# Performance work log

Measured on AMD Instinct MI355X. Metric: run time of the kernel, lower is better.

The kernel has to match this reference:

```python
import jax, jax.numpy as jnp
import numpy as np

BS, N_AGENTS, SA_DIM, HID = 2048, 64, 128, 256


def setup_inputs() -> dict:
    key = jax.random.key(0)
    ks = jax.random.split(key, 16)
    s = lambda fan_in: 1.0 / np.sqrt(fan_in)
    u = lambda k, shp, b: jax.random.uniform(k, shp, jnp.float32, -b, b)
    return {
        "x": jax.random.normal(ks[0], (BS, N_AGENTS, SA_DIM), jnp.float32),
        # encoder: Linear(sa, hid) -> Linear(hid, hid)
        "enc_w1": u(ks[1], (SA_DIM, HID), s(SA_DIM)),
        "enc_b1": u(ks[2], (HID,), s(SA_DIM)),
        "enc_w2": u(ks[3], (HID, HID), s(HID)),
        "enc_b2": u(ks[4], (HID,), s(HID)),
        # attention 'general' linear_in (no bias)
        "attn_w": u(ks[5], (HID, HID), s(HID)),
        # gc1: Linear(sa, hid); nn_gc1: Linear(sa, hid)
        "gc1_w": u(ks[6], (SA_DIM, HID), s(SA_DIM)),
        "gc1_b": u(ks[7], (HID,), s(SA_DIM)),
        "nn1_w": u(ks[8], (SA_DIM, HID), s(SA_DIM)),
        "nn1_b": u(ks[9], (HID,), s(SA_DIM)),
        # gc2: Linear(hid, hid); nn_gc2: Linear(hid, hid)
        "gc2_w": u(ks[10], (HID, HID), s(HID)),
        "gc2_b": u(ks[11], (HID,), s(HID)),
        "nn2_w": u(ks[12], (HID, HID), s(HID)),
        "nn2_b": u(ks[13], (HID,), s(HID)),
        "n_agents": N_AGENTS,
    }


def reference(x, enc_w1, enc_b1, enc_w2, enc_b2, attn_w,
              gc1_w, gc1_b, nn1_w, nn1_b, gc2_w, gc2_b, nn2_w, nn2_b,
              n_agents):
    relu = jax.nn.relu
    inv_n = 1.0 / n_agents
    # encoder MLP: relu(relu(x W1 + b1) W2 + b2)  -> [bs, n, hid]
    emb = relu(relu(x @ enc_w1 + enc_b1) @ enc_w2 + enc_b2)
    # general attention: softmax((emb W_a) emb^T) over last axis -> [bs, n, n]
    scores = jnp.einsum('bnd,bmd->bnm', emb @ attn_w, emb)
    attn = jax.nn.softmax(scores, axis=-1)
    # gc1: adj @ Linear(x); residual relu branch; normalize by n_agents
    feat = relu(jnp.einsum('bnm,bmh->bnh', attn, x @ gc1_w + gc1_b))
    feat = (feat + relu(x @ nn1_w + nn1_b)) * inv_n
    # gc2 on feat
    out = relu(jnp.einsum('bnm,bmh->bnh', attn, feat @ gc2_w + gc2_b))
    out = (out + relu(feat @ nn2_w + nn2_b)) * inv_n
    return out, attn
```

## Files before the change

kernel.cpp:

```cpp
#include <hip/hip_runtime.h>

typedef _Float16 half8 __attribute__((ext_vector_type(8)));
typedef _Float16 half4_t __attribute__((ext_vector_type(4)));
typedef float f32x4 __attribute__((ext_vector_type(4)));

#define NBATCH 2048
#define NA 64
#define SA 128
#define HID 256

#define OFF_X 0
#define OFF_R0 8192
#define OFF_ATT (8192 + 16384)
#define SMEM_BYTES ((8192 + 16384 + 8192) * 2)

#define W_ENC1 0
#define W_ENC2 (W_ENC1 + 128 * 256)
#define W_ATTN (W_ENC2 + 256 * 256)
#define W_GC1 (W_ATTN + 256 * 256)
#define W_NN1 (W_GC1 + 128 * 256)
#define W_GC2 (W_NN1 + 128 * 256)
#define W_NN2 (W_GC2 + 256 * 256)

#define MFMA(a, b, cacc) __builtin_amdgcn_mfma_f32_16x16x32_f16((a), (b), (cacc), 0, 0, 0)

#define BAR()                                            \
  do {                                                   \
    asm volatile("s_waitcnt lgkmcnt(0)" ::: "memory");   \
    __builtin_amdgcn_s_barrier();                        \
  } while (0)

__global__ void pack_all(const float* __restrict__ e1, const float* __restrict__ e2,
                         const float* __restrict__ aw, const float* __restrict__ g1,
                         const float* __restrict__ n1, const float* __restrict__ g2,
                         const float* __restrict__ n2, _Float16* __restrict__ dst) {
  int b = (int)blockIdx.x;
  const float* src;
  int off;
  if (b < 16) { src = e1; off = W_ENC1; }
  else if (b < 48) { src = e2; off = W_ENC2; b -= 16; }
  else if (b < 80) { src = aw; off = W_ATTN; b -= 48; }
  else if (b < 96) { src = g1; off = W_GC1; b -= 80; }
  else if (b < 112) { src = n1; off = W_NN1; b -= 96; }
  else if (b < 144) { src = g2; off = W_GC2; b -= 112; }
  else { src = n2; off = W_NN2; b -= 144; }
  int t = b * 256 + (int)threadIdx.x;
  int lane = t & 63, frag = t >> 6;
  int nt = frag & 15, kt = frag >> 4;
  int g = lane >> 4, c = lane & 15;
  half8 h;
#pragma unroll
  for (int j = 0; j < 8; ++j)
    h[j] = (_Float16)src[(size_t)(kt * 32 + g * 8 + j) * 256 + nt * 16 + c];
  *(half8*)(dst + off + (size_t)t * 8) = h;
}

__global__ __launch_bounds__(256, 2) void dicg_main(
    const float* __restrict__ x, const float* __restrict__ b_enc1,
    const float* __restrict__ b_enc2, const float* __restrict__ b_gc1,
    const float* __restrict__ b_nn1, const float* __restrict__ b_gc2,
    const float* __restrict__ b_nn2, const _Float16* __restrict__ wp,
    float* __restrict__ out, float* __restrict__ attn_out) {
  extern __shared__ _Float16 sm[];
  _Float16* X = sm + OFF_X;
  _Float16* R0 = sm + OFF_R0;
  _Float16* ATTp = sm + OFF_ATT;

  const int tid = (int)threadIdx.x;
  const int wv = tid >> 6;
  const int lane = tid & 63;
  const int g = lane >> 4;
  const int c = lane & 15;
  const int bb = (int)blockIdx.x;
  const float* __restrict__ xb = x + (size_t)bb * (NA * SA);

  auto ldA = [&](const _Float16* p, int kt, int rt) -> half8 {
    return *(const half8*)(p + (kt * 4 + rt) * 512 + lane * 8);
  };
  auto ldB = [&](const _Float16* p, int kt, int ct) -> half8 {
    return *(const half8*)(p + (kt * 16 + ct) * 512 + lane * 8);
  };
  auto wfrag = [&](const _Float16* wb, int kt, int ntg) -> half8 {
    return *(const half8*)(wb + ((size_t)(kt * 16 + ntg) * 64 + lane) * 8);
  };
  auto xfrag = [&](int r0, int k0) -> half8 {
    const float* p = xb + (r0 + c) * SA + k0 + g * 8;
    f32x4 u = *(const f32x4*)p;
    f32x4 v = *(const f32x4*)(p + 4);
    half8 h;
    h[0] = (_Float16)u[0]; h[1] = (_Float16)u[1];
    h[2] = (_Float16)u[2]; h[3] = (_Float16)u[3];
    h[4] = (_Float16)v[0]; h[5] = (_Float16)v[1];
    h[6] = (_Float16)v[2]; h[7] = (_Float16)v[3];
    return h;
  };

  auto stA_val = [&](_Float16* dst, int rt, int nt, int r, float v) {
    int kt = 2 * wv + (nt >> 1);
    int lanep = (2 * (nt & 1) + (c >> 3)) * 16 + 4 * g + r;
    dst[(kt * 4 + rt) * 512 + lanep * 8 + (c & 7)] = (_Float16)v;
  };
  auto ep_storeA = [&](f32x4(&acc)[4][4], const float* bias, bool dorelu) {
#pragma unroll
    for (int nt = 0; nt < 4; ++nt) {
      float bv = bias[64 * wv + 16 * nt + c];
#pragma unroll
      for (int rt = 0; rt < 4; ++rt)
#pragma unroll
        for (int r = 0; r < 4; ++r) {
          float y = acc[rt][nt][r] + bv;
          if (dorelu) y = fmaxf(y, 0.f);
          stA_val(R0, rt, nt, r, y);
        }
    }
  };
  auto ep_storeB = [&](f32x4(&acc)[4][4], const float* bias) {
#pragma unroll
    for (int nt = 0; nt < 4; ++nt) {
      float bv = bias[64 * wv + 16 * nt + c];
#pragma unroll
      for (int rt = 0; rt < 4; ++rt) {
        half4_t h;
#pragma unroll
        for (int r = 0; r < 4; ++r) h[r] = (_Float16)(acc[rt][nt][r] + bv);
        int fi = (rt >> 1) * 16 + 4 * wv + nt;
        int lanep = (2 * (rt & 1) + (g >> 1)) * 16 + c;
        *(half4_t*)(R0 + fi * 512 + lanep * 8 + 4 * (g & 1)) = h;
      }
    }
  };
  auto stQ = [&](const f32x4(&q2)[2], int s) {
    _Float16* base = ATTp + (8 + 2 * wv + s) * 512;
#pragma unroll
    for (int nt2 = 0; nt2 < 2; ++nt2)
#pragma unroll
      for (int r = 0; r < 4; ++r)
        base[((2 * nt2 + (c >> 3)) * 16 + 4 * g + r) * 8 + (c & 7)] = (_Float16)q2[nt2][r];
  };
  auto mm_att = [&](f32x4(&acc)[4][4]) {
#pragma unroll
    for (int kt = 0; kt < 2; ++kt) {
      half8 af[4], bf[4];
#pragma unroll
      for (int rt = 0; rt < 4; ++rt) af[rt] = ldA(ATTp, kt, rt);
#pragma unroll
      for (int nt = 0; nt < 4; ++nt) bf[nt] = ldB(R0, kt, 4 * wv + nt);
#pragma unroll
      for (int rt = 0; rt < 4; ++rt)
#pragma unroll
        for (int nt = 0; nt < 4; ++nt) acc[rt][nt] = MFMA(af[rt], bf[nt], acc[rt][nt]);
    }
  };

  half8 pf2[4][4];
  half8 pfq[8][2];
  half8 pf5g[2][4], pf5n[2][4];
  half8 pf7n[3][4], pf7g[3][4];

  {
    f32x4 acc[4][4]{};
#pragma unroll
    for (int kt = 0; kt < 4; ++kt) {
      half8 af[4], bf[4];
#pragma unroll
      for (int rt = 0; rt < 4; ++rt) af[rt] = xfrag(16 * rt, kt * 32);
#pragma unroll
      for (int nt = 0; nt < 4; ++nt) bf[nt] = wfrag(wp + W_ENC1, kt, 4 * wv + nt);
      if (kt == wv) {
#pragma unroll
        for (int rt = 0; rt < 4; ++rt)
          *(half8*)(X + (kt * 4 + rt) * 512 + lane * 8) = af[rt];
      }
#pragma unroll
      for (int rt = 0; rt < 4; ++rt)
#pragma unroll
        for (int nt = 0; nt < 4; ++nt) acc[rt][nt] = MFMA(af[rt], bf[nt], acc[rt][nt]);
    }
#pragma unroll
    for (int s = 0; s < 4; ++s)
#pragma unroll
      for (int nt = 0; nt < 4; ++nt) pf2[s][nt] = wfrag(wp + W_ENC2, s, 4 * wv + nt);
    ep_storeA(acc, b_enc1, true);
  }
  BAR();
  {
    f32x4 acc[4][4]{};
#pragma unroll
    for (int kt = 0; kt < 8; ++kt) {
      half8 af[4], bf[4];
#pragma unroll
      for (int rt = 0; rt < 4; ++rt) af[rt] = ldA(R0, kt, rt);
#pragma unroll
      for (int nt = 0; nt < 4; ++nt)
        bf[nt] = (kt < 4) ? pf2[kt][nt] : wfrag(wp + W_ENC2, kt, 4 * wv + nt);
#pragma unroll
      for (int rt = 0; rt < 4; ++rt)
#pragma unroll
        for (int nt = 0; nt < 4; ++nt) acc[rt][nt] = MFMA(af[rt], bf[nt], acc[rt][nt]);
    }
#pragma unroll
    for (int k2 = 0; k2 < 8; ++k2) {
      pfq[k2][0] = wfrag(wp + W_ATTN, k2, 0);
      pfq[k2][1] = wfrag(wp + W_ATTN, k2, 1);
    }
    BAR();
    ep_storeA(acc, b_enc2, true);
  }
  BAR();
  {
    half8 aeK[8];
#pragma unroll
    for (int k2 = 0; k2 < 8; ++k2) aeK[k2] = ldA(R0, k2, wv);
    f32x4 sc[4]{};
    {
      f32x4 q2[2]{};
#pragma unroll
      for (int k2 = 0; k2 < 8; ++k2) {
        q2[0] = MFMA(aeK[k2], pfq[k2][0], q2[0]);
        q2[1] = MFMA(aeK[k2], pfq[k2][1], q2[1]);
      }
      stQ(q2, 0);
    }
#pragma unroll
    for (int ktp = 0; ktp < 8; ++ktp) {
      f32x4 q2n[2]{};
      if (ktp < 7) {
#pragma unroll
        for (int k2 = 0; k2 < 8; ++k2) {
          q2n[0] = MFMA(aeK[k2], wfrag(wp + W_ATTN, k2, 2 * ktp + 2), q2n[0]);
          q2n[1] = MFMA(aeK[k2], wfrag(wp + W_ATTN, k2, 2 * ktp + 3), q2n[1]);
        }
      }
      asm volatile("s_waitcnt lgkmcnt(0)" ::: "memory");
      half8 qb = *(const half8*)(ATTp + (8 + 2 * wv + (ktp & 1)) * 512 + lane * 8);
      if (ktp < 7) stQ(q2n, (ktp + 1) & 1);
#pragma unroll
      for (int rt = 0; rt < 4; ++rt) sc[rt] = MFMA(ldA(R0, ktp, rt), qb, sc[rt]);
    }
    float m = sc[0][0];
#pragma unroll
    for (int rt = 0; rt < 4; ++rt)
#pragma unroll
      for (int r = 0; r < 4; ++r) m = fmaxf(m, sc[rt][r]);
    m = fmaxf(m, __shfl_xor(m, 16));
    m = fmaxf(m, __shfl_xor(m, 32));
    float e[4][4], s = 0.f;
#pragma unroll
    for (int rt = 0; rt < 4; ++rt)
#pragma unroll
      for (int r = 0; r < 4; ++r) {
        e[rt][r] = __expf(sc[rt][r] - m);
        s += e[rt][r];
      }
    s += __shfl_xor(s, 16);
    s += __shfl_xor(s, 32);
    float inv = 1.0f / s;
#pragma unroll
    for (int s5 = 0; s5 < 2; ++s5)
#pragma unroll
      for (int nt = 0; nt < 4; ++nt) {
        pf5g[s5][nt] = wfrag(wp + W_GC1, s5, 4 * wv + nt);
        pf5n[s5][nt] = wfrag(wp + W_NN1, s5, 4 * wv + nt);
      }
    float* ao = attn_out + ((size_t)bb * NA + 16 * wv + c) * NA;
#pragma unroll
    for (int rt = 0; rt < 4; ++rt) {
      f32x4 vv;
      half4_t hh;
#pragma unroll
      for (int r = 0; r < 4; ++r) {
        vv[r] = e[rt][r] * inv;
        hh[r] = (_Float16)vv[r];
      }
      *(f32x4*)(ao + 16 * rt + 4 * g) = vv;
      int fi = (rt >> 1) * 4 + wv;
      int lanep = (2 * (rt & 1) + (g >> 1)) * 16 + c;
      *(half4_t*)(ATTp + fi * 512 + lanep * 8 + 4 * (g & 1)) = hh;
    }
  }
  BAR();
  half4_t r1h[4][4];
  {
    f32x4 aG[4][4]{}, aN[4][4]{};
#pragma unroll
    for (int kt = 0; kt < 4; ++kt) {
      half8 af[4], b1[4], b2[4];
#pragma unroll
      for (int rt = 0; rt < 4; ++rt) af[rt] = ldA(X, kt, rt);
#pragma unroll
      for (int nt = 0; nt < 4; ++nt)
        b1[nt] = (kt < 2) ? pf5g[kt][nt] : wfrag(wp + W_GC1, kt, 4 * wv + nt);
#pragma unroll
      for (int nt = 0; nt < 4; ++nt)
        b2[nt] = (kt < 2) ? pf5n[kt][nt] : wfrag(wp + W_NN1, kt, 4 * wv + nt);
#pragma unroll
      for (int rt = 0; rt < 4; ++rt)
#pragma unroll
        for (int nt = 0; nt < 4; ++nt) {
          aG[rt][nt] = MFMA(af[rt], b1[nt], aG[rt][nt]);
          aN[rt][nt] = MFMA(af[rt], b2[nt], aN[rt][nt]);
        }
    }
    ep_storeB(aG, b_gc1);
#pragma unroll
    for (int nt = 0; nt < 4; ++nt) {
      float bv = b_nn1[64 * wv + 16 * nt + c];
#pragma unroll
      for (int rt = 0; rt < 4; ++rt)
#pragma unroll
        for (int r = 0; r < 4; ++r)
          r1h[rt][nt][r] = (_Float16)fmaxf(aN[rt][nt][r] + bv, 0.f);
    }
#pragma unroll
    for (int s2 = 0; s2 < 2; ++s2)
#pragma unroll
      for (int nt = 0; nt < 4; ++nt) {
        pf7n[s2][nt] = wfrag(wp + W_NN2, s2, 4 * wv + nt);
        pf7g[s2][nt] = wfrag(wp + W_GC2, s2, 4 * wv + nt);
      }
  }
  BAR();
  {
#pragma unroll
    for (int nt = 0; nt < 4; ++nt) {
      pf7n[2][nt] = wfrag(wp + W_NN2, 2, 4 * wv + nt);
      pf7g[2][nt] = wfrag(wp + W_GC2, 2, 4 * wv + nt);
    }
    f32x4 a1[4][4]{};
    mm_att(a1);
    BAR();
#pragma unroll
    for (int nt = 0; nt < 4; ++nt)
#pragma unroll
      for (int rt = 0; rt < 4; ++rt)
#pragma unroll
        for (int r = 0; r < 4; ++r)
          stA_val(R0, rt, nt, r,
                  (fmaxf(a1[rt][nt][r], 0.f) + (float)r1h[rt][nt][r]) * 0.015625f);
  }
  BAR();
  half4_t r2h[4][4];
  {
    f32x4 aN2[4][4]{}, aG2[4][4]{};
#pragma unroll
    for (int kt = 0; kt < 8; ++kt) {
      half8 af[4], b1[4], b2[4];
#pragma unroll
      for (int rt = 0; rt < 4; ++rt) af[rt] = ldA(R0, kt, rt);
#pragma unroll
      for (int nt = 0; nt < 4; ++nt)
        b1[nt] = (kt < 3) ? pf7n[kt][nt] : wfrag(wp + W_NN2, kt, 4 * wv + nt);
#pragma unroll
      for (int nt = 0; nt < 4; ++nt)
        b2[nt] = (kt < 3) ? pf7g[kt][nt] : wfrag(wp + W_GC2, kt, 4 * wv + nt);
#pragma unroll
      for (int rt = 0; rt < 4; ++rt)
#pragma unroll
        for (int nt = 0; nt < 4; ++nt) {
          aN2[rt][nt] = MFMA(af[rt], b1[nt], aN2[rt][nt]);
          aG2[rt][nt] = MFMA(af[rt], b2[nt], aG2[rt][nt]);
        }
    }
#pragma unroll
    for (int nt = 0; nt < 4; ++nt) {
      float bv = b_nn2[64 * wv + 16 * nt + c];
#pragma unroll
      for (int rt = 0; rt < 4; ++rt)
#pragma unroll
        for (int r = 0; r < 4; ++r)
          r2h[rt][nt][r] = (_Float16)fmaxf(aN2[rt][nt][r] + bv, 0.f);
    }
    BAR();
    ep_storeB(aG2, b_gc2);
  }
  BAR();
  {
    f32x4 a1[4][4]{};
    mm_att(a1);
    float* ob = out + (size_t)bb * NA * HID;
#pragma unroll
    for (int nt = 0; nt < 4; ++nt)
#pragma unroll
      for (int rt = 0; rt < 4; ++rt)
#pragma unroll
        for (int r = 0; r < 4; ++r)
          ob[(size_t)(16 * rt + 4 * g + r) * HID + 64 * wv + 16 * nt + c] =
              (fmaxf(a1[rt][nt][r], 0.f) + (float)r2h[rt][nt][r]) * 0.015625f;
  }
}

extern "C" void kernel_launch(void* const* d_in, const int* in_sizes, int n_in,
                              void* d_out, int out_size, void* d_ws, size_t ws_size,
                              hipStream_t stream) {
  const float* x = (const float*)d_in[0];
  const float* enc_w1 = (const float*)d_in[1];
  const float* enc_b1 = (const float*)d_in[2];
  const float* enc_w2 = (const float*)d_in[3];
  const float* enc_b2 = (const float*)d_in[4];
  const float* attn_w = (const float*)d_in[5];
  const float* gc1_w = (const float*)d_in[6];
  const float* gc1_b = (const float*)d_in[7];
  const float* nn1_w = (const float*)d_in[8];
  const float* nn1_b = (const float*)d_in[9];
  const float* gc2_w = (const float*)d_in[10];
  const float* gc2_b = (const float*)d_in[11];
  const float* nn2_w = (const float*)d_in[12];
  const float* nn2_b = (const float*)d_in[13];

  _Float16* wp = (_Float16*)d_ws;
  float* out = (float*)d_out;
  float* attn_o = out + (size_t)NBATCH * NA * HID;

  pack_all<<<176, 256, 0, stream>>>(enc_w1, enc_w2, attn_w, gc1_w, nn1_w, gc2_w,
                                    nn2_w, wp);
  dicg_main<<<NBATCH, 256, SMEM_BYTES, stream>>>(
      x, enc_b1, enc_b2, gc1_b, nn1_b, gc2_b, nn2_b, wp, out, attn_o);
}
```

Measured before the change: 154.6 us.

## Compute attention-aggregation outputs transposed to vectorize stores and drop barriers

Swaps MFMA operand order for the gc1/gc2 attention products and the nn residual branches so each lane holds four consecutive hidden columns. Feature tiles can then be written with half4 stores into a transposed LDS layout (read back via a new ldFeat), and the final output uses 16-byte float4 global stores instead of scalar ones. Two block barriers are removed, on the assumption that the new layout lets each wave write only its own region. This aims to cut scattered LDS and global stores and synchronization. It risks read/write races in R0 if the removed barriers were still needed.

Result: no change. 156.3 us (+1.1%).

```diff
diff --git a/kernel.cpp b/kernel.cpp
--- a/kernel.cpp
+++ b/kernel.cpp
@@ -80,6 +80,9 @@
   auto ldB = [&](const _Float16* p, int kt, int ct) -> half8 {
     return *(const half8*)(p + (kt * 16 + ct) * 512 + lane * 8);
   };
+  auto ldFeat = [&](int kt, int rt) -> half8 {
+    return *(const half8*)(R0 + ((kt & 1) * 16 + 4 * (kt >> 1) + rt) * 512 + lane * 8);
+  };
   auto wfrag = [&](const _Float16* wb, int kt, int ntg) -> half8 {
     return *(const half8*)(wb + ((size_t)(kt * 16 + ntg) * 64 + lane) * 8);
   };
@@ -129,6 +132,11 @@
       }
     }
   };
+  auto stFeatT = [&](int nt, int rt, half4_t hv) {
+    int fi = (nt >> 1) * 16 + 4 * wv + rt;
+    int lanep = (2 * (nt & 1) + (g >> 1)) * 16 + c;
+    *(half4_t*)(R0 + fi * 512 + lanep * 8 + 4 * (g & 1)) = hv;
+  };
   auto stQ = [&](const f32x4(&q2)[2], int s) {
     _Float16* base = ATTp + (8 + 2 * wv + s) * 512;
 #pragma unroll
@@ -136,20 +144,6 @@
 #pragma unroll
       for (int r = 0; r < 4; ++r)
         base[((2 * nt2 + (c >> 3)) * 16 + 4 * g + r) * 8 + (c & 7)] = (_Float16)q2[nt2][r];
-  };
-  auto mm_att = [&](f32x4(&acc)[4][4]) {
-#pragma unroll
-    for (int kt = 0; kt < 2; ++kt) {
-      half8 af[4], bf[4];
-#pragma unroll
-      for (int rt = 0; rt < 4; ++rt) af[rt] = ldA(ATTp, kt, rt);
-#pragma unroll
-      for (int nt = 0; nt < 4; ++nt) bf[nt] = ldB(R0, kt, 4 * wv + nt);
-#pragma unroll
-      for (int rt = 0; rt < 4; ++rt)
-#pragma unroll
-        for (int nt = 0; nt < 4; ++nt) acc[rt][nt] = MFMA(af[rt], bf[nt], acc[rt][nt]);
-    }
   };
 
   half8 pf2[4][4];
@@ -298,18 +292,18 @@
 #pragma unroll
         for (int nt = 0; nt < 4; ++nt) {
           aG[rt][nt] = MFMA(af[rt], b1[nt], aG[rt][nt]);
-          aN[rt][nt] = MFMA(af[rt], b2[nt], aN[rt][nt]);
+          aN[nt][rt] = MFMA(b2[nt], af[rt], aN[nt][rt]);
         }
     }
     ep_storeB(aG, b_gc1);
 #pragma unroll
     for (int nt = 0; nt < 4; ++nt) {
-      float bv = b_nn1[64 * wv + 16 * nt + c];
+      f32x4 bv4 = *(const f32x4*)(b_nn1 + 64 * wv + 16 * nt + 4 * g);
 #pragma unroll
       for (int rt = 0; rt < 4; ++rt)
 #pragma unroll
         for (int r = 0; r < 4; ++r)
-          r1h[rt][nt][r] = (_Float16)fmaxf(aN[rt][nt][r] + bv, 0.f);
+          r1h[nt][rt][r] = (_Float16)fmaxf(aN[nt][rt][r] + bv4[r], 0.f);
     }
 #pragma unroll
     for (int s2 = 0; s2 < 2; ++s2)
@@ -319,7 +313,6 @@
         pf7g[s2][nt] = wfrag(wp + W_GC2, s2, 4 * wv + nt);
       }
   }
-  BAR();
   {
 #pragma unroll
     for (int nt = 0; nt < 4; ++nt) {
@@ -327,16 +320,29 @@
       pf7g[2][nt] = wfrag(wp + W_GC2, 2, 4 * wv + nt);
     }
     f32x4 a1[4][4]{};
-    mm_att(a1);
-    BAR();
+#pragma unroll
+    for (int kt = 0; kt < 2; ++kt) {
+      half8 af[4], bf[4];
+#pragma unroll
+      for (int rt = 0; rt < 4; ++rt) af[rt] = ldA(ATTp, kt, rt);
+#pragma unroll
+      for (int nt = 0; nt < 4; ++nt) bf[nt] = ldB(R0, kt, 4 * wv + nt);
+#pragma unroll
+      for (int rt = 0; rt < 4; ++rt)
+#pragma unroll
+        for (int nt = 0; nt < 4; ++nt) a1[nt][rt] = MFMA(bf[nt], af[rt], a1[nt][rt]);
+    }
 #pragma unroll
     for (int nt = 0; nt < 4; ++nt)
 #pragma unroll
-      for (int rt = 0; rt < 4; ++rt)
+      for (int rt = 0; rt < 4; ++rt) {
+        half4_t hv;
 #pragma unroll
         for (int r = 0; r < 4; ++r)
-          stA_val(R0, rt, nt, r,
-                  (fmaxf(a1[rt][nt][r], 0.f) + (float)r1h[rt][nt][r]) * 0.015625f);
+          hv[r] = (_Float16)((fmaxf(a1[nt][rt][r], 0.f) + (float)r1h[nt][rt][r]) *
+                             0.015625f);
+        stFeatT(nt, rt, hv);
+      }
   }
   BAR();
   half4_t r2h[4][4];
@@ -346,7 +352,7 @@
     for (int kt = 0; kt < 8; ++kt) {
       half8 af[4], b1[4], b2[4];
 #pragma unroll
-      for (int rt = 0; rt < 4; ++rt) af[rt] = ldA(R0, kt, rt);
+      for (int rt = 0; rt < 4; ++rt) af[rt] = ldFeat(kt, rt);
 #pragma unroll
       for (int nt = 0; nt < 4; ++nt)
         b1[nt] = (kt < 3) ? pf7n[kt][nt] : wfrag(wp + W_NN2, kt, 4 * wv + nt);
@@ -357,35 +363,47 @@
       for (int rt = 0; rt < 4; ++rt)
 #pragma unroll
         for (int nt = 0; nt < 4; ++nt) {
-          aN2[rt][nt] = MFMA(af[rt], b1[nt], aN2[rt][nt]);
+          aN2[nt][rt] = MFMA(b1[nt], af[rt], aN2[nt][rt]);
           aG2[rt][nt] = MFMA(af[rt], b2[nt], aG2[rt][nt]);
         }
     }
 #pragma unroll
     for (int nt = 0; nt < 4; ++nt) {
-      float bv = b_nn2[64 * wv + 16 * nt + c];
+      f32x4 bv4 = *(const f32x4*)(b_nn2 + 64 * wv + 16 * nt + 4 * g);
 #pragma unroll
       for (int rt = 0; rt < 4; ++rt)
 #pragma unroll
         for (int r = 0; r < 4; ++r)
-          r2h[rt][nt][r] = (_Float16)fmaxf(aN2[rt][nt][r] + bv, 0.f);
+          r2h[nt][rt][r] = (_Float16)fmaxf(aN2[nt][rt][r] + bv4[r], 0.f);
     }
     BAR();
     ep_storeB(aG2, b_gc2);
   }
-  BAR();
   {
     f32x4 a1[4][4]{};
-    mm_att(a1);
+#pragma unroll
+    for (int kt = 0; kt < 2; ++kt) {
+      half8 af[4], bf[4];
+#pragma unroll
+      for (int rt = 0; rt < 4; ++rt) af[rt] = ldA(ATTp, kt, rt);
+#pragma unroll
+      for (int nt = 0; nt < 4; ++nt) bf[nt] = ldB(R0, kt, 4 * wv + nt);
+#pragma unroll
+      for (int rt = 0; rt < 4; ++rt)
+#pragma unroll
+        for (int nt = 0; nt < 4; ++nt) a1[nt][rt] = MFMA(bf[nt], af[rt], a1[nt][rt]);
+    }
     float* ob = out + (size_t)bb * NA * HID;
 #pragma unroll
     for (int nt = 0; nt < 4; ++nt)
 #pragma unroll
-      for (int rt = 0; rt < 4; ++rt)
+      for (int rt = 0; rt < 4; ++rt) {
+        f32x4 vv;
 #pragma unroll
         for (int r = 0; r < 4; ++r)
-          ob[(size_t)(16 * rt + 4 * g + r) * HID + 64 * wv + 16 * nt + c] =
-              (fmaxf(a1[rt][nt][r], 0.f) + (float)r2h[rt][nt][r]) * 0.015625f;
+          vv[r] = (fmaxf(a1[nt][rt][r], 0.f) + (float)r2h[nt][rt][r]) * 0.015625f;
+        *(f32x4*)(ob + (size_t)(16 * rt + c) * HID + 64 * wv + 16 * nt + 4 * g) = vv;
+      }
   }
 }
 
```
